# Performance work log

Hardware: AMD Instinct MI355X
Metric: run time of the kernel (lower is better)

Reference implementation:

```python
import jax, jax.numpy as jnp
import numpy as np

B, L, A, K = 2, 1024, 14, 30
NUM_RBF = 16
NPE = 16  # num_positional_embeddings
EF = 128  # edge_features
EDGE_IN = NPE + NUM_RBF * A * A  # 3152


def setup_inputs() -> dict:
    key = jax.random.key(0)
    ks = jax.random.split(key, 4)
    # coords scaled so pairwise distances span the RBF range [0, 20]
    X = jax.random.normal(ks[0], (B, L, A, 3), dtype=jnp.float32) * 3.0
    mask = jnp.ones((B, L), dtype=jnp.float32)
    residue_idx = jnp.tile(jnp.arange(L, dtype=jnp.int32)[None, :], (B, 1))
    chain_labels = jnp.zeros((B, L), dtype=jnp.int32)
    atom_mask = jax.random.randint(ks[1], (B, L, A), 0, 2).astype(jnp.float32)
    W_edge = jax.random.normal(ks[2], (EF, EDGE_IN), dtype=jnp.float32) * 0.02
    ln_gamma = jnp.ones((EF,), dtype=jnp.float32)
    ln_beta = jnp.zeros((EF,), dtype=jnp.float32)
    return {"X": X, "mask": mask, "residue_idx": residue_idx,
            "chain_labels": chain_labels, "atom_mask": atom_mask,
            "W_edge": W_edge, "ln_gamma": ln_gamma, "ln_beta": ln_beta}


def reference(X, mask, residue_idx, chain_labels, atom_mask, W_edge, ln_gamma, ln_beta):
    Bq, Lq = X.shape[0], X.shape[1]
    # ---- CA pairwise distances + masked top-k (smallest) ----
    X_ca = X[:, :, 1, :]
    m2 = mask[:, :, None] * mask[:, None, :]                    # [B,L,L]
    dX = X_ca[:, :, None, :] - X_ca[:, None, :, :]
    D = m2 * jnp.sqrt(jnp.sum(dX ** 2, -1) + 1e-6)
    D_max = jnp.max(D, -1, keepdims=True)
    D_adjust = D + 2.0 * (1.0 - m2) * D_max
    _, E_idx = jax.lax.top_k(-D_adjust, K)                      # smallest K -> [B,L,K]
    # ---- transformer positional encoding of relative index ----
    ii = jnp.arange(Lq, dtype=jnp.float32)[None, :, None]
    d = (E_idx.astype(jnp.float32) - ii)[..., None]             # [B,L,K,1]
    freq = jnp.exp(jnp.arange(0, NPE, 2, dtype=jnp.float32) * (-(np.log(10000.0) / NPE)))
    angles = d * freq                                           # [B,L,K,NPE/2]
    E_pos = jnp.concatenate([jnp.cos(angles), jnp.sin(angles)], -1)  # [B,L,K,NPE]
    # ---- impute CB, build 14-atom set ----
    N_, Ca, C_, O_ = X[:, :, 0, :], X[:, :, 1, :], X[:, :, 2, :], X[:, :, 3, :]
    b = Ca - N_
    c = C_ - Ca
    a = jnp.cross(b, c)
    Cb = -0.58273431 * a + 0.56802827 * b - 0.54067466 * c + Ca
    X2 = jnp.concatenate([jnp.stack([N_, Ca, C_, O_, Cb], -2), X[:, :, 5:, :]], -2)  # [B,L,14,3]
    am = 1.0 - atom_mask                                        # module passes 1 - atom_mask
    # ---- gather neighbor atoms, fused 14x14 atom-pair RBFs ----
    bidx = jnp.arange(Bq)[:, None, None]
    X2n = X2[bidx, E_idx]                                       # [B,L,K,14,3]
    amn = am[bidx, E_idx]                                       # [B,L,K,14]
    diff = X2[:, :, None, :, None, :] - X2n[:, :, :, None, :, :]
    Dab = jnp.sqrt(jnp.sum(diff ** 2, -1) + 1e-6)               # [B,L,K,14,14] (a of i, b of nbr)
    combo = am[:, :, None, :, None] * amn[:, :, :, None, :]     # [B,L,K,14,14]
    mu = jnp.linspace(0.0, 20.0, NUM_RBF)
    sigma = 20.0 / NUM_RBF
    rbf = jnp.exp(-(((Dab[..., None] - mu) / sigma) ** 2)) * combo[..., None]
    RBF_all = rbf.reshape(Bq, Lq, K, A * A * NUM_RBF)           # matches torch cat order (i,j,rbf)
    # ---- edge embedding + layernorm ----
    E = jnp.concatenate([E_pos, RBF_all], -1)                   # [B,L,K,EDGE_IN]
    E = E @ W_edge.T                                            # [B,L,K,EF]
    mean = jnp.mean(E, -1, keepdims=True)
    var = jnp.var(E, -1, keepdims=True)
    E = (E - mean) / jnp.sqrt(var + 1e-5) * ln_gamma + ln_beta
    return (E, E_idx)
```

## Files before the change

### kernel.cpp

```cpp
#include <hip/hip_runtime.h>
#include <hip/hip_bf16.h>
#include <stdint.h>

#define LQ 1024
#define BQ 2
#define AQ 14
#define KQ 30
#define EFQ 128
#define EDGE_IN 3152
#define KPAD 3200
#define NCHUNK 50
#define MTILE 128
#define ROWS (BQ*LQ*KQ)
#define EIDX_OFF (ROWS*EFQ)

typedef __attribute__((ext_vector_type(8))) _Float16 half8;
typedef __attribute__((ext_vector_type(2))) _Float16 half2t;
typedef __attribute__((ext_vector_type(4))) float floatx4;
typedef unsigned long long ull;

static __device__ __forceinline__ uint32_t pkh(float a, float b) {
    auto h = __builtin_amdgcn_cvt_pkrtz(a, b);
    return __builtin_bit_cast(uint32_t, h);
}
static __device__ __forceinline__ ull umin64(ull a, ull b) { return a < b ? a : b; }

__global__ __launch_bounds__(512) void topk_kernel(
    const float* __restrict__ X, const float* __restrict__ mask,
    const float* __restrict__ W, float* __restrict__ out,
    int* __restrict__ idx_ws, _Float16* __restrict__ wpad)
{
    __shared__ float xs[LQ], ys[LQ], zs[LQ], ms[LQ];
    const int t = threadIdx.x;

    if (blockIdx.x >= 256) {
        int base = (blockIdx.x - 256)*8192 + t;
        #pragma unroll
        for (int r = 0; r < 16; ++r) {
            int idx = base + r*512;
            int n = idx / KPAD, f = idx - n*KPAD;
            float v = (f < EDGE_IN) ? W[(size_t)n*EDGE_IN + f] : 0.0f;
            wpad[idx] = (_Float16)v;
        }
        return;
    }

    const int w = t >> 6, lane = t & 63;
    const int row = blockIdx.x*8 + w;
    const int b = row >> 10, i = row & (LQ - 1);

    for (int j = t; j < LQ; j += 512) {
        size_t base = ((size_t)(b*LQ + j))*42 + 3;
        xs[j] = X[base+0]; ys[j] = X[base+1]; zs[j] = X[base+2];
        ms[j] = mask[b*LQ + j];
    }
    __syncthreads();

    const float mif = ms[i];
    const double cx = (double)xs[i], cy = (double)ys[i], cz = (double)zs[i];

    double Dk[16]; float mf[16];
    bool allone = (mif == 1.0f);
    #pragma unroll
    for (int s = 0; s < 16; ++s) {
        int j = s*64 + lane;
        double dx = __dsub_rn(cx, (double)xs[j]);
        double dy = __dsub_rn(cy, (double)ys[j]);
        double dz = __dsub_rn(cz, (double)zs[j]);
        mf[s] = ms[j];
        Dk[s] = __dadd_rn(__dadd_rn(__dmul_rn(dx,dx), __dmul_rn(dy,dy)),
                          __dmul_rn(dz,dz));
        allone = allone && (mf[s] == 1.0f);
    }

    if (!__all(allone ? 1 : 0)) {
        const double mi_d = (double)mif;
        double lm = 0.0;
        #pragma unroll
        for (int s = 0; s < 16; ++s) {
            double m2 = __dmul_rn(mi_d, (double)mf[s]);
            Dk[s] = __dmul_rn(m2, sqrt(__dadd_rn(Dk[s], 1e-6)));
            lm = fmax(lm, Dk[s]);
        }
        #pragma unroll
        for (int off = 32; off; off >>= 1) lm = fmax(lm, __shfl_xor(lm, off));
        #pragma unroll
        for (int s = 0; s < 16; ++s) {
            double m2 = __dmul_rn(mi_d, (double)mf[s]);
            Dk[s] = __dadd_rn(Dk[s],
                    __dmul_rn(__dmul_rn(2.0, __dsub_rn(1.0, m2)), lm));
        }
    }

    ull key[16];
    #pragma unroll
    for (int s = 0; s < 16; ++s)
        key[s] = (((ull)__double_as_longlong(Dk[s])) & ~1023ull)
               | (unsigned)(s*64 + lane);

    for (int k = 0; k < KQ; ++k) {
        ull a0 = umin64(key[0],  key[1]),  a1 = umin64(key[2],  key[3]);
        ull a2 = umin64(key[4],  key[5]),  a3 = umin64(key[6],  key[7]);
        ull a4 = umin64(key[8],  key[9]),  a5 = umin64(key[10], key[11]);
        ull a6 = umin64(key[12], key[13]), a7 = umin64(key[14], key[15]);
        ull b0 = umin64(a0, a1), b1 = umin64(a2, a3);
        ull b2 = umin64(a4, a5), b3 = umin64(a6, a7);
        ull bk = umin64(umin64(b0, b1), umin64(b2, b3));
        #pragma unroll
        for (int off = 32; off; off >>= 1)
            bk = umin64(bk, (ull)__shfl_xor(bk, off));
        int j = (int)(bk & 1023ull);
        if (lane == 0) {
            int rg = row*KQ + k;
            idx_ws[rg] = j;
            out[EIDX_OFF + rg] = (float)j;
        }
        bool mine = ((j & 63) == lane);
        int s_win = j >> 6;
        #pragma unroll
        for (int s = 0; s < 16; ++s)
            key[s] = (mine && s == s_win) ? ~0ull : key[s];
    }
}

struct FusedSmem {
    alignas(16) unsigned short atoms[256*56];
    alignas(16) unsigned short Bl[128*64];
    alignas(16) float drow[MTILE];
    int residg[256];
    unsigned int maskb[256];
    float gsh[EFQ], bsh[EFQ];
};

static __device__ __forceinline__ void gen8(
    const unsigned short* __restrict__ atomsA,
    const unsigned short* __restrict__ atomsB,
    unsigned maskA, unsigned maskB, float drowv,
    int f0, uint32_t* __restrict__ v)
{
    if (f0 >= 16) {
        int p = (f0 - 16) >> 4;
        if (p >= AQ*AQ) { v[0] = v[1] = v[2] = v[3] = 0u; return; }
        int rbase = (f0 - 16) & 15;
        int a  = (p * 74899) >> 20;
        int bp = p - a*14;
        bool czero = ((((maskA >> a) | (maskB >> bp)) & 1u) != 0u);
        half2t c0 = *reinterpret_cast<const half2t*>(atomsA + a*4);
        half2t c1 = *reinterpret_cast<const half2t*>(atomsA + a*4 + 2);
        half2t n0 = *reinterpret_cast<const half2t*>(atomsB + bp*4);
        half2t n1 = *reinterpret_cast<const half2t*>(atomsB + bp*4 + 2);
        half2t dxy = c0 - n0;
        half2t dzw = c1 - n1;
        float dx = (float)dxy[0], dy = (float)dxy[1], dz = (float)dzw[0];
        float u = __builtin_amdgcn_sqrtf(dx*dx + dy*dy + dz*dz + 1e-6f) * 0.96089846f;
        float e[8];
        #pragma unroll
        for (int j = 0; j < 8; ++j) {
            float tt = __fmaf_rn(-(float)(rbase + j), 1.28119795f, u);
            e[j] = __builtin_amdgcn_exp2f(-(tt*tt));
        }
        #pragma unroll
        for (int k = 0; k < 4; ++k) v[k] = czero ? 0u : pkh(e[2*k], e[2*k+1]);
    } else {
        const float fr[8] = {1.0f, 0.31622776601683794f, 0.1f,
            0.031622776601683794f, 0.01f, 0.0031622776601683794f,
            0.001f, 0.00031622776601683794f};
        float e[8];
        if (f0 == 0) {
            #pragma unroll
            for (int j = 0; j < 8; ++j) e[j] = __cosf(drowv * fr[j]);
        } else {
            #pragma unroll
            for (int j = 0; j < 8; ++j) e[j] = __sinf(drowv * fr[j]);
        }
        #pragma unroll
        for (int k = 0; k < 4; ++k) v[k] = pkh(e[2*k], e[2*k+1]);
    }
}

__global__ __launch_bounds__(512) void fused_kernel(
    const float* __restrict__ X, const float* __restrict__ atom_mask,
    const _Float16* __restrict__ wpad, const float* __restrict__ gamma,
    const float* __restrict__ beta, const int* __restrict__ idx_ws,
    float* __restrict__ out)
{
    __shared__ FusedSmem sm;
    const int t = threadIdx.x;
    const int row0 = blockIdx.x * MTILE;
    const int b = row0 / (LQ*KQ);

    if (t < MTILE) {
        int rg = row0 + t;
        int rem = rg - b*(LQ*KQ);
        int i = rem / KQ;
        int j = idx_ws[rg];
        sm.residg[t]       = b*LQ + i;
        sm.residg[MTILE+t] = b*LQ + j;
        sm.drow[t] = (float)j - (float)i;
    }
    if (t < EFQ) { sm.gsh[t] = gamma[t]; sm.bsh[t] = beta[t]; }
    __syncthreads();

    for (int u = t; u < 256*14; u += 512) {
        int s = u / 14; int a = u - s*14;
        const float* xp = X + (size_t)sm.residg[s]*42 + a*3;
        uint2 pk; pk.x = pkh(xp[0], xp[1]); pk.y = pkh(xp[2], 0.0f);
        *reinterpret_cast<uint2*>(&sm.atoms[s*56 + a*4]) = pk;
    }
    __syncthreads();

    if (t < 256) {
        unsigned short* at = &sm.atoms[t*56];
        auto ld3 = [&](int slot, float& x, float& y, float& z) {
            half2t p0 = *reinterpret_cast<const half2t*>(at + slot*4);
            half2t p1 = *reinterpret_cast<const half2t*>(at + slot*4 + 2);
            x = (float)p0[0]; y = (float)p0[1]; z = (float)p1[0];
        };
        float Nx,Ny,Nz, Cax,Cay,Caz, Cx,Cy,Cz;
        ld3(0, Nx,Ny,Nz); ld3(1, Cax,Cay,Caz); ld3(2, Cx,Cy,Cz);
        float bx=Cax-Nx, by=Cay-Ny, bz=Caz-Nz;
        float ex=Cx-Cax, ey=Cy-Cay, ez=Cz-Caz;
        float ax = by*ez - bz*ey, ay = bz*ex - bx*ez, az = bx*ey - by*ex;
        float cbx = -0.58273431f*ax + 0.56802827f*bx - 0.54067466f*ex + Cax;
        float cby = -0.58273431f*ay + 0.56802827f*by - 0.54067466f*ey + Cay;
        float cbz = -0.58273431f*az + 0.56802827f*bz - 0.54067466f*ez + Caz;
        uint2 pk; pk.x = pkh(cbx, cby); pk.y = pkh(cbz, 0.0f);
        *reinterpret_cast<uint2*>(at + 4*4) = pk;
        unsigned mb = 0;
        const float* amp = &atom_mask[(size_t)sm.residg[t]*AQ];
        #pragma unroll
        for (int a = 0; a < AQ; ++a) if (amp[a] > 0.5f) mb |= (1u << a);
        sm.maskb[t] = mb;
    }

    const int w = t >> 6, lane = t & 63, q = lane >> 4, l15 = lane & 15;
    const int m = w*16 + l15;

    int boff0[8], boff1[8];
    #pragma unroll
    for (int nt = 0; nt < 8; ++nt) {
        int n = nt*16 + l15;
        boff0[nt] = n*64 + ((q ^ (n&7))*8);
        boff1[nt] = n*64 + (((4+q) ^ (n&7))*8);
    }
    int stRegion[2]; const _Float16* stBase[2];
    #pragma unroll
    for (int i2 = 0; i2 < 2; ++i2) {
        int region = w*2 + i2;
        int n = region*8 + (lane >> 3);
        int kbsrc = (lane & 7) ^ (lane >> 3);
        stRegion[i2] = region;
        stBase[i2] = wpad + (size_t)n*KPAD + kbsrc*8;
    }
    auto stage = [&](int c) {
        #pragma unroll
        for (int i2 = 0; i2 < 2; ++i2) {
            const _Float16* g = stBase[i2] + c*64;
            __builtin_amdgcn_global_load_lds(
                (const __attribute__((address_space(1))) uint32_t*)g,
                (__attribute__((address_space(3))) uint32_t*)&sm.Bl[stRegion[i2]*512],
                16, 0, 0);
        }
    };

    floatx4 acc[8];
    #pragma unroll
    for (int nt = 0; nt < 8; ++nt) acc[nt] = (floatx4){0.f,0.f,0.f,0.f};

    __syncthreads();

    const unsigned short* atomsA = &sm.atoms[m*56];
    const unsigned short* atomsB = &sm.atoms[(MTILE+m)*56];
    const unsigned maskA = sm.maskb[m], maskB = sm.maskb[MTILE+m];
    const float drowv = sm.drow[m];

    union H8 { uint32_t u[4]; half8 h; };
    for (int c = 0; c < NCHUNK; ++c) {
        if (c) __syncthreads();
        stage(c);
        H8 va0, va1;
        gen8(atomsA, atomsB, maskA, maskB, drowv, c*64 + q*8,      va0.u);
        gen8(atomsA, atomsB, maskA, maskB, drowv, c*64 + 32 + q*8, va1.u);
        __syncthreads();
        #pragma unroll
        for (int nt = 0; nt < 8; ++nt) {
            half8 b0 = *reinterpret_cast<const half8*>(&sm.Bl[boff0[nt]]);
            half8 b1 = *reinterpret_cast<const half8*>(&sm.Bl[boff1[nt]]);
            acc[nt] = __builtin_amdgcn_mfma_f32_16x16x32_f16(va0.h, b0, acc[nt], 0, 0, 0);
            acc[nt] = __builtin_amdgcn_mfma_f32_16x16x32_f16(va1.h, b1, acc[nt], 0, 0, 0);
        }
    }

    #pragma unroll
    for (int v = 0; v < 4; ++v) {
        float s = 0.f, s2 = 0.f;
        #pragma unroll
        for (int nt = 0; nt < 8; ++nt) { float x = acc[nt][v]; s += x; s2 += x*x; }
        #pragma unroll
        for (int off = 1; off < 16; off <<= 1) {
            s  += __shfl_xor(s,  off);
            s2 += __shfl_xor(s2, off);
        }
        float mean = s * (1.0f/128.0f);
        float var  = s2 * (1.0f/128.0f) - mean*mean;
        float rstd = 1.0f / sqrtf(var + 1e-5f);
        int row_l = w*16 + q*4 + v;
        size_t obase = (size_t)(row0 + row_l)*EFQ;
        #pragma unroll
        for (int nt = 0; nt < 8; ++nt) {
            int col = nt*16 + l15;
            out[obase + col] = (acc[nt][v] - mean)*rstd*sm.gsh[col] + sm.bsh[col];
        }
    }
}

extern "C" void kernel_launch(void* const* d_in, const int* in_sizes, int n_in,
                              void* d_out, int out_size, void* d_ws, size_t ws_size,
                              hipStream_t stream)
{
    const float* X         = (const float*)d_in[0];
    const float* mask      = (const float*)d_in[1];
    const float* atom_mask = (const float*)d_in[4];
    const float* W         = (const float*)d_in[5];
    const float* gamma     = (const float*)d_in[6];
    const float* beta      = (const float*)d_in[7];
    float* out = (float*)d_out;

    int*       idx_ws = (int*)d_ws;
    _Float16*  wpad   = (_Float16*)((char*)d_ws + 262144);

    hipLaunchKernelGGL(topk_kernel, dim3(306), dim3(512), 0, stream,
                       X, mask, W, out, idx_ws, wpad);
    hipLaunchKernelGGL(fused_kernel, dim3(ROWS/MTILE), dim3(512), 0, stream,
                       X, atom_mask, wpad, gamma, beta, idx_ws, out);
}
```

Before: 175.7 us.

## Halve block to 256 threads with two 16-row MFMA tiles per wave

```diff
diff --git a/kernel.cpp b/kernel.cpp
--- a/kernel.cpp
+++ b/kernel.cpp
@@ -140,11 +140,12 @@
 {
     if (f0 >= 16) {
         int p = (f0 - 16) >> 4;
-        if (p >= AQ*AQ) { v[0] = v[1] = v[2] = v[3] = 0u; return; }
         int rbase = (f0 - 16) & 15;
-        int a  = (p * 74899) >> 20;
-        int bp = p - a*14;
-        bool czero = ((((maskA >> a) | (maskB >> bp)) & 1u) != 0u);
+        int pc = p > 195 ? 195 : p;
+        int a  = (pc * 74899) >> 20;
+        int bp = pc - a*14;
+        bool dead = (p > 195) |
+                    ((((maskA >> a) | (maskB >> bp)) & 1u) != 0u);
         half2t c0 = *reinterpret_cast<const half2t*>(atomsA + a*4);
         half2t c1 = *reinterpret_cast<const half2t*>(atomsA + a*4 + 2);
         half2t n0 = *reinterpret_cast<const half2t*>(atomsB + bp*4);
@@ -153,14 +154,14 @@
         half2t dzw = c1 - n1;
         float dx = (float)dxy[0], dy = (float)dxy[1], dz = (float)dzw[0];
         float u = __builtin_amdgcn_sqrtf(dx*dx + dy*dy + dz*dz + 1e-6f) * 0.96089846f;
-        float e[8];
-        #pragma unroll
-        for (int j = 0; j < 8; ++j) {
-            float tt = __fmaf_rn(-(float)(rbase + j), 1.28119795f, u);
-            e[j] = __builtin_amdgcn_exp2f(-(tt*tt));
-        }
-        #pragma unroll
-        for (int k = 0; k < 4; ++k) v[k] = czero ? 0u : pkh(e[2*k], e[2*k+1]);
+        u = dead ? 1.0e4f : u;
+        #pragma unroll
+        for (int k = 0; k < 4; ++k) {
+            float t0 = __fmaf_rn(-(float)(rbase + 2*k),     1.28119795f, u);
+            float t1 = __fmaf_rn(-(float)(rbase + 2*k + 1), 1.28119795f, u);
+            v[k] = pkh(__builtin_amdgcn_exp2f(-(t0*t0)),
+                       __builtin_amdgcn_exp2f(-(t1*t1)));
+        }
     } else {
         const float fr[8] = {1.0f, 0.31622776601683794f, 0.1f,
             0.031622776601683794f, 0.01f, 0.0031622776601683794f,
@@ -178,7 +179,7 @@
     }
 }
 
-__global__ __launch_bounds__(512) void fused_kernel(
+__global__ __launch_bounds__(256, 3) void fused_kernel(
     const float* __restrict__ X, const float* __restrict__ atom_mask,
     const _Float16* __restrict__ wpad, const float* __restrict__ gamma,
     const float* __restrict__ beta, const int* __restrict__ idx_ws,
@@ -201,15 +202,15 @@
     if (t < EFQ) { sm.gsh[t] = gamma[t]; sm.bsh[t] = beta[t]; }
     __syncthreads();
 
-    for (int u = t; u < 256*14; u += 512) {
-        int s = u / 14; int a = u - s*14;
+    for (int u2 = t; u2 < 256*14; u2 += 256) {
+        int s = u2 / 14; int a = u2 - s*14;
         const float* xp = X + (size_t)sm.residg[s]*42 + a*3;
         uint2 pk; pk.x = pkh(xp[0], xp[1]); pk.y = pkh(xp[2], 0.0f);
         *reinterpret_cast<uint2*>(&sm.atoms[s*56 + a*4]) = pk;
     }
     __syncthreads();
 
-    if (t < 256) {
+    {
         unsigned short* at = &sm.atoms[t*56];
         auto ld3 = [&](int slot, float& x, float& y, float& z) {
             half2t p0 = *reinterpret_cast<const half2t*>(at + slot*4);
@@ -234,84 +235,92 @@
     }
 
     const int w = t >> 6, lane = t & 63, q = lane >> 4, l15 = lane & 15;
-    const int m = w*16 + l15;
-
-    int boff0[8], boff1[8];
+    const int m0 = w*32 + l15, m1 = m0 + 16;
+
+    const int cst0 = l15*64 + ((q ^ (l15 & 7))*8);
+    const int cst1 = l15*64 + (((4+q) ^ (l15 & 7))*8);
+
+    const _Float16* stBase[4];
+    unsigned short* stDst[4];
+    #pragma unroll
+    for (int i2 = 0; i2 < 4; ++i2) {
+        int region = w*4 + i2;
+        int n = region*8 + (lane >> 3);
+        int kbsrc = (lane & 7) ^ (lane >> 3);
+        stDst[i2]  = &sm.Bl[region*512];
+        stBase[i2] = wpad + (size_t)n*KPAD + kbsrc*8;
+    }
+
+    floatx4 acc0[8], acc1[8];
     #pragma unroll
     for (int nt = 0; nt < 8; ++nt) {
-        int n = nt*16 + l15;
-        boff0[nt] = n*64 + ((q ^ (n&7))*8);
-        boff1[nt] = n*64 + (((4+q) ^ (n&7))*8);
-    }
-    int stRegion[2]; const _Float16* stBase[2];
-    #pragma unroll
-    for (int i2 = 0; i2 < 2; ++i2) {
-        int region = w*2 + i2;
-        int n = region*8 + (lane >> 3);
-        int kbsrc = (lane & 7) ^ (lane >> 3);
-        stRegion[i2] = region;
-        stBase[i2] = wpad + (size_t)n*KPAD + kbsrc*8;
-    }
-    auto stage = [&](int c) {
-        #pragma unroll
-        for (int i2 = 0; i2 < 2; ++i2) {
+        acc0[nt] = (floatx4){0.f,0.f,0.f,0.f};
+        acc1[nt] = (floatx4){0.f,0.f,0.f,0.f};
+    }
+
+    __syncthreads();
+
+    const unsigned short* atomsA0 = &sm.atoms[m0*56];
+    const unsigned short* atomsB0 = &sm.atoms[(MTILE+m0)*56];
+    const unsigned short* atomsA1 = &sm.atoms[m1*56];
+    const unsigned short* atomsB1 = &sm.atoms[(MTILE+m1)*56];
+    const unsigned maskA0 = sm.maskb[m0], maskB0 = sm.maskb[MTILE+m0];
+    const unsigned maskA1 = sm.maskb[m1], maskB1 = sm.maskb[MTILE+m1];
+    const float drow0 = sm.drow[m0], drow1 = sm.drow[m1];
+
+    union H8 { uint32_t u[4]; half8 h; };
+    for (int c = 0; c < NCHUNK; ++c) {
+        if (c) __syncthreads();
+        #pragma unroll
+        for (int i2 = 0; i2 < 4; ++i2) {
             const _Float16* g = stBase[i2] + c*64;
             __builtin_amdgcn_global_load_lds(
                 (const __attribute__((address_space(1))) uint32_t*)g,
-                (__attribute__((address_space(3))) uint32_t*)&sm.Bl[stRegion[i2]*512],
+                (__attribute__((address_space(3))) uint32_t*)stDst[i2],
                 16, 0, 0);
         }
+        H8 a00, a01, a10, a11;
+        gen8(atomsA0, atomsB0, maskA0, maskB0, drow0, c*64 + q*8,      a00.u);
+        gen8(atomsA0, atomsB0, maskA0, maskB0, drow0, c*64 + 32 + q*8, a01.u);
+        gen8(atomsA1, atomsB1, maskA1, maskB1, drow1, c*64 + q*8,      a10.u);
+        gen8(atomsA1, atomsB1, maskA1, maskB1, drow1, c*64 + 32 + q*8, a11.u);
+        __syncthreads();
+        #pragma unroll
+        for (int nt = 0; nt < 8; ++nt) {
+            half8 b0 = *reinterpret_cast<const half8*>(&sm.Bl[nt*1024 + cst0]);
+            half8 b1 = *reinterpret_cast<const half8*>(&sm.Bl[nt*1024 + cst1]);
+            acc0[nt] = __builtin_amdgcn_mfma_f32_16x16x32_f16(a00.h, b0, acc0[nt], 0, 0, 0);
+            acc0[nt] = __builtin_amdgcn_mfma_f32_16x16x32_f16(a01.h, b1, acc0[nt], 0, 0, 0);
+            acc1[nt] = __builtin_amdgcn_mfma_f32_16x16x32_f16(a10.h, b0, acc1[nt], 0, 0, 0);
+            acc1[nt] = __builtin_amdgcn_mfma_f32_16x16x32_f16(a11.h, b1, acc1[nt], 0, 0, 0);
+        }
+    }
+
+    auto lnrows = [&](const floatx4* acc, int gbase) {
+        #pragma unroll
+        for (int v = 0; v < 4; ++v) {
+            float s = 0.f, s2 = 0.f;
+            #pragma unroll
+            for (int nt = 0; nt < 8; ++nt) { float x = acc[nt][v]; s += x; s2 += x*x; }
+            #pragma unroll
+            for (int off = 1; off < 16; off <<= 1) {
+                s  += __shfl_xor(s,  off);
+                s2 += __shfl_xor(s2, off);
+            }
+            float mean = s * (1.0f/128.0f);
+            float var  = s2 * (1.0f/128.0f) - mean*mean;
+            float rstd = 1.0f / sqrtf(var + 1e-5f);
+            int row_l = w*32 + gbase + q*4 + v;
+            size_t obase = (size_t)(row0 + row_l)*EFQ;
+            #pragma unroll
+            for (int nt = 0; nt < 8; ++nt) {
+                int col = nt*16 + l15;
+                out[obase + col] = (acc[nt][v] - mean)*rstd*sm.gsh[col] + sm.bsh[col];
+            }
+        }
     };
-
-    floatx4 acc[8];
-    #pragma unroll
-    for (int nt = 0; nt < 8; ++nt) acc[nt] = (floatx4){0.f,0.f,0.f,0.f};
-
-    __syncthreads();
-
-    const unsigned short* atomsA = &sm.atoms[m*56];
-    const unsigned short* atomsB = &sm.atoms[(MTILE+m)*56];
-    const unsigned maskA = sm.maskb[m], maskB = sm.maskb[MTILE+m];
-    const float drowv = sm.drow[m];
-
-    union H8 { uint32_t u[4]; half8 h; };
-    for (int c = 0; c < NCHUNK; ++c) {
-        if (c) __syncthreads();
-        stage(c);
-        H8 va0, va1;
-        gen8(atomsA, atomsB, maskA, maskB, drowv, c*64 + q*8,      va0.u);
-        gen8(atomsA, atomsB, maskA, maskB, drowv, c*64 + 32 + q*8, va1.u);
-        __syncthreads();
-        #pragma unroll
-        for (int nt = 0; nt < 8; ++nt) {
-            half8 b0 = *reinterpret_cast<const half8*>(&sm.Bl[boff0[nt]]);
-            half8 b1 = *reinterpret_cast<const half8*>(&sm.Bl[boff1[nt]]);
-            acc[nt] = __builtin_amdgcn_mfma_f32_16x16x32_f16(va0.h, b0, acc[nt], 0, 0, 0);
-            acc[nt] = __builtin_amdgcn_mfma_f32_16x16x32_f16(va1.h, b1, acc[nt], 0, 0, 0);
-        }
-    }
-
-    #pragma unroll
-    for (int v = 0; v < 4; ++v) {
-        float s = 0.f, s2 = 0.f;
-        #pragma unroll
-        for (int nt = 0; nt < 8; ++nt) { float x = acc[nt][v]; s += x; s2 += x*x; }
-        #pragma unroll
-        for (int off = 1; off < 16; off <<= 1) {
-            s  += __shfl_xor(s,  off);
-            s2 += __shfl_xor(s2, off);
-        }
-        float mean = s * (1.0f/128.0f);
-        float var  = s2 * (1.0f/128.0f) - mean*mean;
-        float rstd = 1.0f / sqrtf(var + 1e-5f);
-        int row_l = w*16 + q*4 + v;
-        size_t obase = (size_t)(row0 + row_l)*EFQ;
-        #pragma unroll
-        for (int nt = 0; nt < 8; ++nt) {
-            int col = nt*16 + l15;
-            out[obase + col] = (acc[nt][v] - mean)*rstd*sm.gsh[col] + sm.bsh[col];
-        }
-    }
+    lnrows(acc0, 0);
+    lnrows(acc1, 16);
 }
 
 extern "C" void kernel_launch(void* const* d_in, const int* in_sizes, int n_in,
@@ -331,6 +340,6 @@
 
     hipLaunchKernelGGL(topk_kernel, dim3(306), dim3(512), 0, stream,
                        X, mask, W, out, idx_ws, wpad);
-    hipLaunchKernelGGL(fused_kernel, dim3(ROWS/MTILE), dim3(512), 0, stream,
+    hipLaunchKernelGGL(fused_kernel, dim3(ROWS/MTILE), dim3(256), 0, stream,
                        X, atom_mask, wpad, gamma, beta, idx_ws, out);
 }
```

Measured after the change: 177.7 us. No clear change (+1.2%).

## Double-buffer weight chunks and pre-bake atom masking into coordinates

Applied to the files above, without the earlier changes.

```diff
diff --git a/kernel.cpp b/kernel.cpp
--- a/kernel.cpp
+++ b/kernel.cpp
@@ -125,56 +125,36 @@
 
 struct FusedSmem {
     alignas(16) unsigned short atoms[256*56];
-    alignas(16) unsigned short Bl[128*64];
+    alignas(16) unsigned short Bl[2*8192];
     alignas(16) float drow[MTILE];
     int residg[256];
-    unsigned int maskb[256];
     float gsh[EFQ], bsh[EFQ];
 };
 
-static __device__ __forceinline__ void gen8(
-    const unsigned short* __restrict__ atomsA,
-    const unsigned short* __restrict__ atomsB,
-    unsigned maskA, unsigned maskB, float drowv,
-    int f0, uint32_t* __restrict__ v)
+static __device__ __forceinline__ void gen_rbf(
+    const char* __restrict__ rowA, const char* __restrict__ rowB,
+    int ao, int bo, float rboff, uint32_t* __restrict__ v)
 {
-    if (f0 >= 16) {
-        int p = (f0 - 16) >> 4;
-        if (p >= AQ*AQ) { v[0] = v[1] = v[2] = v[3] = 0u; return; }
-        int rbase = (f0 - 16) & 15;
-        int a  = (p * 74899) >> 20;
-        int bp = p - a*14;
-        bool czero = ((((maskA >> a) | (maskB >> bp)) & 1u) != 0u);
-        half2t c0 = *reinterpret_cast<const half2t*>(atomsA + a*4);
-        half2t c1 = *reinterpret_cast<const half2t*>(atomsA + a*4 + 2);
-        half2t n0 = *reinterpret_cast<const half2t*>(atomsB + bp*4);
-        half2t n1 = *reinterpret_cast<const half2t*>(atomsB + bp*4 + 2);
-        half2t dxy = c0 - n0;
-        half2t dzw = c1 - n1;
-        float dx = (float)dxy[0], dy = (float)dxy[1], dz = (float)dzw[0];
-        float u = __builtin_amdgcn_sqrtf(dx*dx + dy*dy + dz*dz + 1e-6f) * 0.96089846f;
-        float e[8];
-        #pragma unroll
-        for (int j = 0; j < 8; ++j) {
-            float tt = __fmaf_rn(-(float)(rbase + j), 1.28119795f, u);
-            e[j] = __builtin_amdgcn_exp2f(-(tt*tt));
-        }
-        #pragma unroll
-        for (int k = 0; k < 4; ++k) v[k] = czero ? 0u : pkh(e[2*k], e[2*k+1]);
-    } else {
-        const float fr[8] = {1.0f, 0.31622776601683794f, 0.1f,
-            0.031622776601683794f, 0.01f, 0.0031622776601683794f,
-            0.001f, 0.00031622776601683794f};
-        float e[8];
-        if (f0 == 0) {
-            #pragma unroll
-            for (int j = 0; j < 8; ++j) e[j] = __cosf(drowv * fr[j]);
-        } else {
-            #pragma unroll
-            for (int j = 0; j < 8; ++j) e[j] = __sinf(drowv * fr[j]);
-        }
-        #pragma unroll
-        for (int k = 0; k < 4; ++k) v[k] = pkh(e[2*k], e[2*k+1]);
+    uint2 ca = *reinterpret_cast<const uint2*>(rowA + ao);
+    uint2 nb = *reinterpret_cast<const uint2*>(rowB + bo);
+    half2t c0 = __builtin_bit_cast(half2t, ca.x);
+    half2t c1 = __builtin_bit_cast(half2t, ca.y);
+    half2t n0 = __builtin_bit_cast(half2t, nb.x);
+    half2t n1 = __builtin_bit_cast(half2t, nb.y);
+    half2t dxy = c0 - n0;
+    half2t dzw = c1 - n1;
+    float dx = (float)dxy[0], dy = (float)dxy[1], dz = (float)dzw[0];
+    float ssq = __fmaf_rn(dx, dx, __fmaf_rn(dy, dy,
+                __fmaf_rn(dz, dz, 9.2332585e-7f)));
+    float u = __builtin_amdgcn_sqrtf(ssq) + rboff;
+    const float CJ[8] = {0.0f, 1.28119795f, 2.5623959f, 3.84359385f,
+                         5.1247918f, 6.40598975f, 7.6871877f, 8.96838565f};
+    #pragma unroll
+    for (int k = 0; k < 4; ++k) {
+        float t0 = u - CJ[2*k];
+        float t1 = u - CJ[2*k+1];
+        v[k] = pkh(__builtin_amdgcn_exp2f(-(t0*t0)),
+                   __builtin_amdgcn_exp2f(-(t1*t1)));
     }
 }
 
@@ -201,8 +181,33 @@
     if (t < EFQ) { sm.gsh[t] = gamma[t]; sm.bsh[t] = beta[t]; }
     __syncthreads();
 
-    for (int u = t; u < 256*14; u += 512) {
-        int s = u / 14; int a = u - s*14;
+    const int w = t >> 6, lane = t & 63, q = lane >> 4, l15 = lane & 15;
+    const int m = w*16 + l15;
+
+    int stRegion[2]; const _Float16* stBase[2];
+    #pragma unroll
+    for (int i2 = 0; i2 < 2; ++i2) {
+        int region = w*2 + i2;
+        int n = region*8 + (lane >> 3);
+        int kbsrc = (lane & 7) ^ (lane >> 3);
+        stRegion[i2] = region;
+        stBase[i2] = wpad + (size_t)n*KPAD + kbsrc*8;
+    }
+    auto stage = [&](int c) {
+        #pragma unroll
+        for (int i2 = 0; i2 < 2; ++i2) {
+            const _Float16* g = stBase[i2] + c*64;
+            __builtin_amdgcn_global_load_lds(
+                (const __attribute__((address_space(1))) uint32_t*)g,
+                (__attribute__((address_space(3))) uint32_t*)
+                    &sm.Bl[((c & 1) << 13) + stRegion[i2]*512],
+                16, 0, 0);
+        }
+    };
+    stage(0);
+
+    for (int u2 = t; u2 < 256*14; u2 += 512) {
+        int s = u2 / 14; int a = u2 - s*14;
         const float* xp = X + (size_t)sm.residg[s]*42 + a*3;
         uint2 pk; pk.x = pkh(xp[0], xp[1]); pk.y = pkh(xp[2], 0.0f);
         *reinterpret_cast<uint2*>(&sm.atoms[s*56 + a*4]) = pk;
@@ -224,17 +229,25 @@
         float cbx = -0.58273431f*ax + 0.56802827f*bx - 0.54067466f*ex + Cax;
         float cby = -0.58273431f*ay + 0.56802827f*by - 0.54067466f*ey + Cay;
         float cbz = -0.58273431f*az + 0.56802827f*bz - 0.54067466f*ez + Caz;
-        uint2 pk; pk.x = pkh(cbx, cby); pk.y = pkh(cbz, 0.0f);
-        *reinterpret_cast<uint2*>(at + 4*4) = pk;
-        unsigned mb = 0;
+        uint2 pk4; pk4.x = pkh(cbx, cby); pk4.y = pkh(cbz, 0.0f);
+        *reinterpret_cast<uint2*>(at + 4*4) = pk4;
+
+        const float P = (t < MTILE) ? 30000.0f : -30000.0f;
+        const uint32_t pxx = pkh(P, P), pxy = pkh(P, 0.0f);
+        half2t sc2; sc2[0] = (_Float16)0.96089846f; sc2[1] = (_Float16)0.96089846f;
         const float* amp = &atom_mask[(size_t)sm.residg[t]*AQ];
         #pragma unroll
-        for (int a = 0; a < AQ; ++a) if (amp[a] > 0.5f) mb |= (1u << a);
-        sm.maskb[t] = mb;
-    }
-
-    const int w = t >> 6, lane = t & 63, q = lane >> 4, l15 = lane & 15;
-    const int m = w*16 + l15;
+        for (int a = 0; a < AQ; ++a) {
+            uint2 vv = *reinterpret_cast<const uint2*>(at + a*4);
+            half2t lo = __builtin_bit_cast(half2t, vv.x) * sc2;
+            half2t hi = __builtin_bit_cast(half2t, vv.y) * sc2;
+            bool msk = amp[a] > 0.5f;
+            uint2 ov;
+            ov.x = msk ? pxx : __builtin_bit_cast(uint32_t, lo);
+            ov.y = msk ? pxy : __builtin_bit_cast(uint32_t, hi);
+            *reinterpret_cast<uint2*>(at + a*4) = ov;
+        }
+    }
 
     int boff0[8], boff1[8];
     #pragma unroll
@@ -243,52 +256,63 @@
         boff0[nt] = n*64 + ((q ^ (n&7))*8);
         boff1[nt] = n*64 + (((4+q) ^ (n&7))*8);
     }
-    int stRegion[2]; const _Float16* stBase[2];
-    #pragma unroll
-    for (int i2 = 0; i2 < 2; ++i2) {
-        int region = w*2 + i2;
-        int n = region*8 + (lane >> 3);
-        int kbsrc = (lane & 7) ^ (lane >> 3);
-        stRegion[i2] = region;
-        stBase[i2] = wpad + (size_t)n*KPAD + kbsrc*8;
-    }
-    auto stage = [&](int c) {
-        #pragma unroll
-        for (int i2 = 0; i2 < 2; ++i2) {
-            const _Float16* g = stBase[i2] + c*64;
-            __builtin_amdgcn_global_load_lds(
-                (const __attribute__((address_space(1))) uint32_t*)g,
-                (__attribute__((address_space(3))) uint32_t*)&sm.Bl[stRegion[i2]*512],
-                16, 0, 0);
-        }
-    };
+
+    const char* rowA = (const char*)&sm.atoms[m*56];
+    const char* rowB = (const char*)&sm.atoms[(MTILE+m)*56];
+    const int   qlt2  = (q < 2) ? 1 : 0;
+    const float rboff = -(float)((q & 1) * 8) * 1.28119795f;
 
     floatx4 acc[8];
     #pragma unroll
     for (int nt = 0; nt < 8; ++nt) acc[nt] = (floatx4){0.f,0.f,0.f,0.f};
 
     __syncthreads();
-
-    const unsigned short* atomsA = &sm.atoms[m*56];
-    const unsigned short* atomsB = &sm.atoms[(MTILE+m)*56];
-    const unsigned maskA = sm.maskb[m], maskB = sm.maskb[MTILE+m];
-    const float drowv = sm.drow[m];
 
     union H8 { uint32_t u[4]; half8 h; };
     for (int c = 0; c < NCHUNK; ++c) {
-        if (c) __syncthreads();
-        stage(c);
-        H8 va0, va1;
-        gen8(atomsA, atomsB, maskA, maskB, drowv, c*64 + q*8,      va0.u);
-        gen8(atomsA, atomsB, maskA, maskB, drowv, c*64 + 32 + q*8, va1.u);
+        if (c < NCHUNK-1) stage(c+1);
+
+        int p0 = 4*c - qlt2;
+        int p1 = p0 + 2;
+        int pa0 = (p0 * 74899) >> 20;  int pa1 = (p1 * 74899) >> 20;
+        pa0 = pa0 > 13 ? 13 : pa0;     pa1 = pa1 > 13 ? 13 : pa1;
+        int ao0 = pa0 << 3, bo0 = (p0 - pa0*14) << 3;
+        int ao1 = pa1 << 3, bo1 = (p1 - pa1*14) << 3;
+
+        H8 a00, a01;
+        if (c == 0) {
+            if (qlt2) {
+                const float fr[8] = {1.0f, 0.31622776601683794f, 0.1f,
+                    0.031622776601683794f, 0.01f, 0.0031622776601683794f,
+                    0.001f, 0.00031622776601683794f};
+                float dr = sm.drow[m];
+                float e[8];
+                if (q == 0) {
+                    #pragma unroll
+                    for (int j = 0; j < 8; ++j) e[j] = __cosf(dr * fr[j]);
+                } else {
+                    #pragma unroll
+                    for (int j = 0; j < 8; ++j) e[j] = __sinf(dr * fr[j]);
+                }
+                #pragma unroll
+                for (int k = 0; k < 4; ++k) a00.u[k] = pkh(e[2*k], e[2*k+1]);
+            } else {
+                gen_rbf(rowA, rowB, ao0, bo0, rboff, a00.u);
+            }
+        } else {
+            gen_rbf(rowA, rowB, ao0, bo0, rboff, a00.u);
+        }
+        gen_rbf(rowA, rowB, ao1, bo1, rboff, a01.u);
+
+        const unsigned short* Bb = &sm.Bl[(c & 1) << 13];
+        #pragma unroll
+        for (int nt = 0; nt < 8; ++nt) {
+            half8 b0 = *reinterpret_cast<const half8*>(&Bb[boff0[nt]]);
+            half8 b1 = *reinterpret_cast<const half8*>(&Bb[boff1[nt]]);
+            acc[nt] = __builtin_amdgcn_mfma_f32_16x16x32_f16(a00.h, b0, acc[nt], 0, 0, 0);
+            acc[nt] = __builtin_amdgcn_mfma_f32_16x16x32_f16(a01.h, b1, acc[nt], 0, 0, 0);
+        }
         __syncthreads();
-        #pragma unroll
-        for (int nt = 0; nt < 8; ++nt) {
-            half8 b0 = *reinterpret_cast<const half8*>(&sm.Bl[boff0[nt]]);
-            half8 b1 = *reinterpret_cast<const half8*>(&sm.Bl[boff1[nt]]);
-            acc[nt] = __builtin_amdgcn_mfma_f32_16x16x32_f16(va0.h, b0, acc[nt], 0, 0, 0);
-            acc[nt] = __builtin_amdgcn_mfma_f32_16x16x32_f16(va1.h, b1, acc[nt], 0, 0, 0);
-        }
     }
 
     #pragma unroll
```

After: 169.3 us, median of 2. 1.04x faster.
